# Performance work log

Measured on AMD Instinct MI355X. Metric: run time of the kernel, lower is better.

## Reference

```python
import jax, jax.numpy as jnp
import numpy as np

N_QUBITS = 7
N_LAYERS = 2
DIM = 2 ** N_QUBITS  # 128
NORM_FACTOR = 1.0


def _cnot_gather_idx(n):
    # CNOT chain (0,1),(1,2),...,(n-2,n-1) plus wraparound (n-1,0).
    # new_state[x] = old_state[idx[x]]; apply gates in reverse to arange.
    gates = [(i, i + 1) for i in range(n - 1)] + [(n - 1, 0)]
    idx = np.arange(2 ** n)
    for c, t in reversed(gates):
        cbit = 1 << (n - 1 - c)  # pennylane wire 0 = most significant bit
        tbit = 1 << (n - 1 - t)
        idx = np.where((idx & cbit) > 0, idx ^ tbit, idx)
    return jnp.asarray(idx)

CNOT_IDX = _cnot_gather_idx(N_QUBITS)


def silu(x):
    return x * jax.nn.sigmoid(x)


def cayley(A_real, A_imag):
    # Hermitianize then Cayley transform -> unitary, per layer. [L,D,D]
    A = A_real.astype(jnp.complex64) + 1j * A_imag.astype(jnp.complex64)
    A = A + jnp.conj(jnp.swapaxes(A, -1, -2))
    I = jnp.eye(DIM, dtype=A.dtype)
    return jnp.matmul(A - 1j * I, jnp.linalg.inv(A + 1j * I))


def _single_qubit_gate(theta_x, theta_y):
    # combined G = RY(theta_y) @ RX(theta_x) applied to every qubit
    cx, sx = jnp.cos(theta_x / 2), jnp.sin(theta_x / 2)
    cy, sy = jnp.cos(theta_y / 2), jnp.sin(theta_y / 2)
    RX = jnp.stack([jnp.stack([cx + 0j, -1j * sx]), jnp.stack([-1j * sx, cx + 0j])])
    RY = jnp.stack([jnp.stack([cy + 0j, -sy + 0j]), jnp.stack([sy + 0j, cy + 0j])])
    return RY @ RX


def quantum_evolve(psi, coeffs, q_mats):
    # psi: [N, DIM] complex64 normalized state vectors
    N = psi.shape[0]
    for j in range(N_LAYERS):
        psi = psi @ q_mats[j].T  # QubitUnitary: new = U @ old
        G = _single_qubit_gate(coeffs[j, 0], coeffs[j, 1])
        psi = psi.reshape((N,) + (2,) * N_QUBITS)
        for ax in range(1, N_QUBITS + 1):
            psi = jnp.moveaxis(jnp.tensordot(G, psi, axes=((1,), (ax,))), 0, ax)
        psi = psi.reshape(N, DIM)
        psi = psi[:, CNOT_IDX]  # CNOT chain is a fixed basis permutation
    return psi


def setup_inputs() -> dict:
    key = jax.random.key(0)
    ks = jax.random.split(key, 16)
    N, E = 50000, 800000
    in_nf, hid, out_nf = 128, 128, 128
    h = jax.random.normal(ks[0], (N, in_nf), dtype=jnp.float32)
    edge_index = jax.random.randint(ks[1], (2, E), 0, N)
    s = 0.05
    W_e1 = jax.random.normal(ks[2], (2 * in_nf, hid), dtype=jnp.float32) * s
    b_e1 = jnp.zeros((hid,), dtype=jnp.float32)
    W_e2 = jax.random.normal(ks[3], (hid, hid), dtype=jnp.float32) * s
    b_e2 = jnp.zeros((hid,), dtype=jnp.float32)
    W_enc = jax.random.normal(ks[4], (hid + in_nf, DIM), dtype=jnp.float32) * s
    b_enc = jnp.zeros((DIM,), dtype=jnp.float32)
    coeffs = jax.random.normal(ks[5], (N_LAYERS, 2), dtype=jnp.float32) * 0.1
    A_real = jax.random.normal(ks[6], (N_LAYERS, DIM, DIM), dtype=jnp.float32) * 0.01
    A_imag = jax.random.normal(ks[7], (N_LAYERS, DIM, DIM), dtype=jnp.float32) * 0.01
    W_dec = jax.random.normal(ks[8], (DIM, out_nf), dtype=jnp.float32) * s
    b_dec = jnp.zeros((out_nf,), dtype=jnp.float32)
    return {"h": h, "edge_index": edge_index, "W_e1": W_e1, "b_e1": b_e1,
            "W_e2": W_e2, "b_e2": b_e2, "W_enc": W_enc, "b_enc": b_enc,
            "coeffs": coeffs, "A_real": A_real, "A_imag": A_imag,
            "W_dec": W_dec, "b_dec": b_dec}


def reference(h, edge_index, W_e1, b_e1, W_e2, b_e2, W_enc, b_enc,
              coeffs, A_real, A_imag, W_dec, b_dec):
    row, col = edge_index[0], edge_index[1]
    # edge model: mij = MLP([h_src, h_tgt])
    e = jnp.concatenate([h[row], h[col]], axis=1)  # [E, 2*in_nf]
    e = silu(e @ W_e1 + b_e1)
    edge_feat = silu(e @ W_e2 + b_e2)  # [E, hid]
    # node model: scatter-sum aggregation over destination `row`
    agg = jax.ops.segment_sum(edge_feat, row, num_segments=h.shape[0]) / NORM_FACTOR
    q_input = jnp.concatenate([h, agg], axis=1) @ W_enc + b_enc  # [N, DIM]
    norm = jnp.sqrt(jnp.sum(q_input ** 2, axis=1, keepdims=True) + 1e-12)
    psi = (q_input / norm).astype(jnp.complex64)
    q_mats = cayley(A_real, A_imag)  # [L, DIM, DIM] unitary
    psi = quantum_evolve(psi, coeffs, q_mats)
    out = h + (jnp.real(psi) @ W_dec + b_dec)
    return out, edge_feat
```

## Files before the change

### kernel.cpp

```cpp
#include <hip/hip_runtime.h>
#include <math.h>

#define N_NODES 50000
#define N_EDGES 800000

typedef __attribute__((ext_vector_type(8))) short bf16x8;
typedef __attribute__((ext_vector_type(4))) short bf16x4;
typedef __attribute__((ext_vector_type(2))) short shortx2;
typedef __attribute__((ext_vector_type(4))) float f32x4;

__device__ __forceinline__ float silu_f(float x) {
    float d = 1.0f + __expf(-x);
    return x * __builtin_amdgcn_rcpf(d);
}

__device__ __forceinline__ unsigned short f2bf(float x) {
    union { float f; unsigned u; } v; v.f = x;
    unsigned r = v.u + 0x7FFFu + ((v.u >> 16) & 1u);
    return (unsigned short)(r >> 16);
}

__device__ __forceinline__ void atomic_pk_add_bf16(short* addr, shortx2 v) {
    typedef shortx2 __attribute__((address_space(1)))* gp1;
    __builtin_amdgcn_global_atomic_fadd_v2bf16((gp1)(unsigned long long)addr, v);
}

__global__ __launch_bounds__(256) void prep_kernel(const float* __restrict__ h,
                                                   short* __restrict__ hbf,
                                                   const int* __restrict__ ei,
                                                   int* __restrict__ cnt,
                                                   const float* __restrict__ A_real,
                                                   const float* __restrict__ A_imag,
                                                   float* __restrict__ H,
                                                   float* __restrict__ X) {
    const int bid = blockIdx.x;
    const int t = threadIdx.x;
    if (bid < 3125) {
        int i = bid * 256 + t;
        const float4* h4 = (const float4*)h;
        float4 v0 = h4[i * 2], v1 = h4[i * 2 + 1];
        bf16x8 b;
        b[0] = (short)f2bf(v0.x); b[1] = (short)f2bf(v0.y);
        b[2] = (short)f2bf(v0.z); b[3] = (short)f2bf(v0.w);
        b[4] = (short)f2bf(v1.x); b[5] = (short)f2bf(v1.y);
        b[6] = (short)f2bf(v1.z); b[7] = (short)f2bf(v1.w);
        ((bf16x8*)hbf)[i] = b;
        atomicAdd(&cnt[ei[i]], 1);
    } else {
        int p = bid - 3125;
        int L = p >> 2, q4 = p & 3;
        const float* ar = A_real + L * 16384;
        const float* ai = A_imag + L * 16384;
        float* hre = H + L * 32768;
        float* him = hre + 16384;
        float* xre = X + L * 32768;
        float* xim = xre + 16384;
        for (int m = 0; m < 16; ++m) {
            int idx = q4 * 4096 + t + 256 * m;
            int i = idx >> 7, j = idx & 127;
            float hr = ar[idx] + ar[j * 128 + i];
            float hi = ai[idx] - ai[j * 128 + i];
            hre[idx] = hr;
            him[idx] = hi;
            xre[idx] = hr;
            xim[idx] = hi - (i == j ? 1.0f : 0.0f);
        }
    }
}

__device__ __forceinline__ void ns_t_body(int blk, int t,
                                          const float* __restrict__ H,
                                          const float* __restrict__ X,
                                          float* __restrict__ T) {
    const int L = blk >> 4;
    const int i = (blk & 15) * 8 + (t >> 7);
    const int j = t & 127;
    const float* hre = H + L * 32768;
    const float* him = hre + 16384;
    const float* xre = X + L * 32768;
    const float* xim = xre + 16384;
    float accr = 0.f, acci = 0.f;
    #pragma unroll 4
    for (int k = 0; k < 128; ++k) {
        float hr = hre[i * 128 + k], hi = him[i * 128 + k];
        float xr = xre[k * 128 + j], xi = xim[k * 128 + j];
        accr += hr * xr - hi * xi;
        acci += hr * xi + hi * xr;
    }
    T[L * 32768 + i * 128 + j]          = accr - xim[i * 128 + j];
    T[L * 32768 + 16384 + i * 128 + j]  = acci + xre[i * 128 + j];
}

__device__ __forceinline__ void ns_x_body(int blk, int t,
                                          const float* __restrict__ X,
                                          const float* __restrict__ T,
                                          float* __restrict__ Xout) {
    const int L = blk >> 4;
    const int i = (blk & 15) * 8 + (t >> 7);
    const int j = t & 127;
    const float* xre = X + L * 32768;
    const float* xim = xre + 16384;
    const float* tre = T + L * 32768;
    const float* tim = tre + 16384;
    float accr = 0.f, acci = 0.f;
    #pragma unroll 4
    for (int k = 0; k < 128; ++k) {
        float xr = xre[i * 128 + k], xi = xim[i * 128 + k];
        float tr = tre[k * 128 + j], ti = tim[k * 128 + j];
        accr += xr * tr - xi * ti;
        acci += xr * ti + xi * tr;
    }
    Xout[L * 32768 + i * 128 + j]          = 2.0f * xre[i * 128 + j] - accr;
    Xout[L * 32768 + 16384 + i * 128 + j]  = 2.0f * xim[i * 128 + j] - acci;
}

__global__ __launch_bounds__(1024) void nst_scan_kernel(const float* __restrict__ H,
                                                        const float* __restrict__ X,
                                                        float* __restrict__ T,
                                                        const int* __restrict__ cnt,
                                                        int* __restrict__ cursor) {
    const int bid = blockIdx.x;
    const int t = threadIdx.x;
    if (bid < 32) { ns_t_body(bid, t, H, X, T); return; }
    __shared__ int sA[1024];
    __shared__ int sB[1024];
    const int CH = 49;
    int s = 0;
    #pragma unroll 4
    for (int i = 0; i < CH; ++i) {
        int idx = t * CH + i;
        if (idx < N_NODES) s += cnt[idx];
    }
    sA[t] = s;
    __syncthreads();
    int* src = sA;
    int* dst = sB;
    for (int off = 1; off < 1024; off <<= 1) {
        int v = src[t];
        if (t >= off) v += src[t - off];
        dst[t] = v;
        __syncthreads();
        int* tmp = src; src = dst; dst = tmp;
    }
    int run = (t == 0) ? 0 : src[t - 1];
    for (int i = 0; i < CH; ++i) {
        int idx = t * CH + i;
        if (idx < N_NODES) {
            cursor[idx] = run;
            run += cnt[idx];
        }
    }
}

__global__ __launch_bounds__(1024) void fill_nsx_kernel(const int* __restrict__ ei,
                                                        int* __restrict__ cursor,
                                                        int* __restrict__ elist,
                                                        const float* __restrict__ X,
                                                        const float* __restrict__ T,
                                                        float* __restrict__ Xout) {
    const int bid = blockIdx.x;
    const int t = threadIdx.x;
    if (bid < 782) {
        int e = bid * 1024 + t;
        if (e < N_EDGES) {
            int slot = atomicAdd(&cursor[ei[e]], 1);
            elist[slot] = e;
        }
        return;
    }
    ns_x_body(bid - 782, t, X, T, Xout);
}

__global__ __launch_bounds__(1024) void ns_t_kernel(const float* __restrict__ H,
                                                    const float* __restrict__ X,
                                                    float* __restrict__ T) {
    ns_t_body(blockIdx.x, threadIdx.x, H, X, T);
}

__global__ __launch_bounds__(1024) void ns_x_kernel(const float* __restrict__ X,
                                                    const float* __restrict__ T,
                                                    float* __restrict__ Xout) {
    ns_x_body(blockIdx.x, threadIdx.x, X, T, Xout);
}

__global__ __launch_bounds__(1024) void gateperm_kernel(const float* __restrict__ X,
                                                        const float* __restrict__ coeffs,
                                                        float* __restrict__ Y) {
    __shared__ float Mre[128 * 129];
    __shared__ float Mim[128 * 129];
    const int L = blockIdx.x;
    const int t = threadIdx.x;
    const float* xre = X + L * 32768;
    const float* xim = xre + 16384;

    for (int q = 0; q < 16; ++q) {
        int idx = t + 1024 * q;
        int i = idx >> 7, j = idx & 127;
        Mre[i * 129 + j] = (i == j ? 1.0f : 0.0f) + 2.0f * xim[idx];
        Mim[i * 129 + j] = -2.0f * xre[idx];
    }
    __syncthreads();

    const float tx = coeffs[2 * L + 0] * 0.5f;
    const float ty = coeffs[2 * L + 1] * 0.5f;
    const float cx = cosf(tx), sx = sinf(tx), cy = cosf(ty), sy = sinf(ty);
    const float G00r = cx * cy, G00i = sx * sy;
    const float G01r = -cx * sy, G01i = -sx * cy;
    const float G10r = cx * sy, G10i = -sx * cy;
    const float G11r = cx * cy, G11i = -sx * sy;

    for (int st = 0; st < 7; ++st) {
        int b = 1 << st;
        #pragma unroll
        for (int p = 0; p < 8; ++p) {
            int pid = t + 1024 * p;
            int col = pid & 127, ph = pid >> 7;
            int i0 = ((ph >> st) << (st + 1)) | (ph & (b - 1));
            int i1 = i0 | b;
            float v0r = Mre[i0 * 129 + col], v0i = Mim[i0 * 129 + col];
            float v1r = Mre[i1 * 129 + col], v1i = Mim[i1 * 129 + col];
            Mre[i0 * 129 + col] = G00r * v0r - G00i * v0i + G01r * v1r - G01i * v1i;
            Mim[i0 * 129 + col] = G00r * v0i + G00i * v0r + G01r * v1i + G01i * v1r;
            Mre[i1 * 129 + col] = G10r * v0r - G10i * v0i + G11r * v1r - G11i * v1i;
            Mim[i1 * 129 + col] = G10r * v0i + G10i * v0r + G11r * v1i + G11i * v1r;
        }
        __syncthreads();
    }

    const int cs[7] = {6, 5, 4, 3, 2, 1, 0};
    const int ts[7] = {0, 6, 5, 4, 3, 2, 1};
    float* yre = Y + L * 32768;
    float* yim = yre + 16384;
    for (int q = 0; q < 16; ++q) {
        int idx = t + 1024 * q;
        int ii_ = idx >> 7, col = idx & 127;
        int s = ii_;
        #pragma unroll
        for (int m = 0; m < 7; ++m) {
            int cbit = 1 << (6 - cs[m]);
            int tbit = 1 << (6 - ts[m]);
            if (s & cbit) s ^= tbit;
        }
        yre[idx] = Mre[s * 129 + col];
        yim[idx] = Mim[s * 129 + col];
    }
}

__global__ __launch_bounds__(512) void combine1_kernel(const float* __restrict__ Y,
                                                       float* __restrict__ ReM) {
    __shared__ float q1r[16384];
    __shared__ float q1i[16384];
    const int t = threadIdx.x;
    const float* q1re = Y;
    const float* q1im = Y + 16384;
    const float* q2re = Y + 32768;
    const float* q2im = Y + 49152;
    for (int q = 0; q < 32; ++q) {
        q1r[t + 512 * q] = q1re[t + 512 * q];
        q1i[t + 512 * q] = q1im[t + 512 * q];
    }
    __syncthreads();
    int i = blockIdx.x * 4 + (t >> 7);
    int j = t & 127;
    float acc = 0.f;
    for (int k = 0; k < 128; ++k) {
        acc += q2re[i * 128 + k] * q1r[k * 128 + j] - q2im[i * 128 + k] * q1i[k * 128 + j];
    }
    ReM[i * 128 + j] = acc;
}

__global__ __launch_bounds__(512) void combine2_kernel(const float* __restrict__ ReM,
                                                       const float* __restrict__ W_dec,
                                                       short* __restrict__ Dt) {
    __shared__ float ml[16384];
    __shared__ float wl[16384];
    const int t = threadIdx.x;
    for (int q = 0; q < 32; ++q) {
        ml[t + 512 * q] = ReM[t + 512 * q];
        wl[t + 512 * q] = W_dec[t + 512 * q];
    }
    __syncthreads();
    int k = blockIdx.x * 4 + (t >> 7);
    int j = t & 127;
    float acc = 0.f;
    for (int i = 0; i < 128; ++i) {
        acc += ml[i * 128 + k] * wl[i * 128 + j];
    }
    Dt[j * 128 + k] = (short)f2bf(acc);
}

__global__ __launch_bounds__(768)
__attribute__((amdgpu_waves_per_eu(3, 3)))
void edge_kernel(const short* __restrict__ hbf,
                 const int* __restrict__ ei,
                 const int* __restrict__ elist,
                 const float* __restrict__ W_e1,
                 const float* __restrict__ b_e1,
                 const float* __restrict__ W_e2,
                 const float* __restrict__ b_e2,
                 float* __restrict__ ef_out,
                 short* __restrict__ agg_bf) {
    __shared__ short w1f[64 * 64 * 8];
    __shared__ short w2f[32 * 64 * 8];
    __shared__ short c1s[12][16 * 68];

    const int t = threadIdx.x;
    const int lane = t & 63;
    const int w = t >> 6;
    const int l15 = lane & 15;
    const int kg = lane >> 4;

    {
        const float4* w1_4 = (const float4*)W_e1;
        for (int idx4 = t; idx4 < 8192; idx4 += 768) {
            int k = idx4 >> 5, j4 = idx4 & 31;
            float4 v = w1_4[idx4];
            int s = k >> 5, kgs = (k >> 3) & 3, e = k & 7;
            int fb = s * 8;
            float vz[4] = {v.x, v.y, v.z, v.w};
            #pragma unroll
            for (int z = 0; z < 4; ++z) {
                int j = j4 * 4 + z;
                int nf = j >> 4, jl = j & 15;
                w1f[((fb + nf) * 64 + kgs * 16 + jl) * 8 + e] = (short)f2bf(vz[z]);
            }
        }
        const float4* w2_4 = (const float4*)W_e2;
        for (int idx4 = t; idx4 < 4096; idx4 += 768) {
            int k = idx4 >> 5, j4 = idx4 & 31;
            float4 v = w2_4[idx4];
            int s2 = k >> 5, kgs = (k >> 3) & 3, e = k & 7;
            int fb = s2 * 8;
            float vz[4] = {v.x, v.y, v.z, v.w};
            #pragma unroll
            for (int z = 0; z < 4; ++z) {
                int j = j4 * 4 + z;
                int nf = j >> 4, jl = j & 15;
                w2f[((fb + nf) * 64 + kgs * 16 + jl) * 8 + e] = (short)f2bf(vz[z]);
            }
        }
    }
    float b1v[8], b2v[8];
    #pragma unroll
    for (int nf = 0; nf < 8; ++nf) {
        b1v[nf] = b_e1[nf * 16 + l15];
        b2v[nf] = b_e2[nf * 16 + l15];
    }
    __syncthreads();

    const bf16x8* hb8 = (const bf16x8*)hbf;
    const bf16x8* w1v = (const bf16x8*)w1f;
    const bf16x8* w2v = (const bf16x8*)w2f;
    short* myc1 = &c1s[w][0];
    const int nt = N_EDGES / 16;
    const int TW = gridDim.x * 12;
    const int wvid = blockIdx.x * 12 + w;
    int tile = (int)(((long long)nt * wvid) / TW);
    const int tend = (int)(((long long)nt * (wvid + 1)) / TW);
    if (tile >= tend) return;

    int el = elist[tile * 16 + l15];
    int ri = ei[el];
    int ci = ei[N_EDGES + el];
    bf16x8 a1[8];
    #pragma unroll
    for (int s = 0; s < 4; ++s) a1[s] = hb8[(size_t)ri * 16 + s * 4 + kg];
    #pragma unroll
    for (int s = 0; s < 4; ++s) a1[4 + s] = hb8[(size_t)ci * 16 + s * 4 + kg];

    bool hn = (tile + 1 < tend);
    int eln = 0, rin = 0, cin = 0;
    if (hn) {
        eln = elist[(tile + 1) * 16 + l15];
        rin = ei[eln];
        cin = ei[N_EDGES + eln];
    }

    float runsum[8];
    #pragma unroll
    for (int nf = 0; nf < 8; ++nf) runsum[nf] = 0.f;

    for (;;) {
        bool hn2 = (tile + 2 < tend);
        int eln2 = 0, rin2 = 0, cin2 = 0;
        if (hn2) {
            eln2 = elist[(tile + 2) * 16 + l15];
            rin2 = ei[eln2];
            cin2 = ei[N_EDGES + eln2];
        }

        f32x4 acc[8];
        #pragma unroll
        for (int nf = 0; nf < 8; ++nf) acc[nf] = (f32x4){0.f, 0.f, 0.f, 0.f};
        __builtin_amdgcn_s_setprio(1);
        #pragma unroll
        for (int s = 0; s < 8; ++s) {
            #pragma unroll
            for (int nf = 0; nf < 8; ++nf) {
                bf16x8 b = w1v[(s * 8 + nf) * 64 + lane];
                acc[nf] = __builtin_amdgcn_mfma_f32_16x16x32_bf16(a1[s], b, acc[nf], 0, 0, 0);
            }
        }
        __builtin_amdgcn_s_setprio(0);

        bf16x8 a1n[8];
        if (hn) {
            #pragma unroll
            for (int s = 0; s < 4; ++s) a1n[s] = hb8[(size_t)rin * 16 + s * 4 + kg];
            #pragma unroll
            for (int s = 0; s < 4; ++s) a1n[4 + s] = hb8[(size_t)cin * 16 + s * 4 + kg];
        }

        f32x4 acc2[8];
        #pragma unroll
        for (int nf = 0; nf < 8; ++nf) acc2[nf] = (f32x4){0.f, 0.f, 0.f, 0.f};
        #pragma unroll
        for (int half = 0; half < 2; ++half) {
            #pragma unroll
            for (int nfh = 0; nfh < 4; ++nfh) {
                int nf = half * 4 + nfh;
                #pragma unroll
                for (int r = 0; r < 4; ++r) {
                    int row = kg * 4 + r;
                    int c = nfh * 16 + l15;
                    myc1[row * 68 + c] = (short)f2bf(silu_f(acc[nf][r] + b1v[nf]));
                }
            }
            #pragma unroll
            for (int s2l = 0; s2l < 2; ++s2l) {
                int k0h = s2l * 32 + kg * 8;
                int base = l15 * 68 + k0h;
                bf16x4 lo = *(const bf16x4*)&myc1[base];
                bf16x4 hi = *(const bf16x4*)&myc1[base + 4];
                bf16x8 a2;
                #pragma unroll
                for (int z = 0; z < 4; ++z) { a2[z] = lo[z]; a2[4 + z] = hi[z]; }
                int s2 = half * 2 + s2l;
                __builtin_amdgcn_s_setprio(1);
                #pragma unroll
                for (int nf = 0; nf < 8; ++nf) {
                    bf16x8 b = w2v[(s2 * 8 + nf) * 64 + lane];
                    acc2[nf] = __builtin_amdgcn_mfma_f32_16x16x32_bf16(a2, b, acc2[nf], 0, 0, 0);
                }
                __builtin_amdgcn_s_setprio(0);
            }
        }

        int rw[4], ew[4];
        #pragma unroll
        for (int r = 0; r < 4; ++r) {
            rw[r] = __shfl(ri, kg * 4 + r);
            ew[r] = __shfl(el, kg * 4 + r);
        }
        int rwn0 = hn ? __shfl(rin, kg * 4) : -1;
        #pragma unroll
        for (int r = 0; r < 4; ++r) {
            float* efp = ef_out + (size_t)ew[r] * 128;
            #pragma unroll
            for (int nf = 0; nf < 8; ++nf) {
                int col = nf * 16 + l15;
                float v = silu_f(acc2[nf][r] + b2v[nf]);
                __builtin_nontemporal_store(v, efp + col);
                runsum[nf] += v;
            }
            bool end = (r < 3) ? (rw[r + 1] != rw[r]) : (rw[3] != rwn0);
            if (end) {
                short* agp = agg_bf + (size_t)rw[r] * 128;
                #pragma unroll
                for (int nf = 0; nf < 8; ++nf) {
                    float vn = __shfl_xor(runsum[nf], 1);
                    if ((l15 & 1) == 0) {
                        shortx2 pk;
                        pk.x = (short)f2bf(runsum[nf]);
                        pk.y = (short)f2bf(vn);
                        atomic_pk_add_bf16(agp + nf * 16 + l15, pk);
                    }
                    runsum[nf] = 0.f;
                }
            }
        }

        if (!hn) break;
        tile += 1;
        el = eln; ri = rin; ci = cin;
        #pragma unroll
        for (int s = 0; s < 8; ++s) a1[s] = a1n[s];
        hn = hn2; eln = eln2; rin = rin2; cin = cin2;
    }
}

__global__ __launch_bounds__(1024)
__attribute__((amdgpu_waves_per_eu(4, 4)))
void node_kernel(const short* __restrict__ hbf,
                 const short* __restrict__ agg_bf,
                 const float* __restrict__ W_enc,
                 const float* __restrict__ b_enc,
                 const short* __restrict__ Dt_bf,
                 const float* __restrict__ b_dec,
                 const float* __restrict__ h,
                 float* __restrict__ out) {
    __shared__ short wef[64 * 64 * 8];
    __shared__ short dtf[32 * 64 * 8];
    __shared__ short c1s[16][16 * 68];

    const int t = threadIdx.x;
    const int lane = t & 63;
    const int w = t >> 6;
    const int l15 = lane & 15;
    const int kg = lane >> 4;

    {
        const float4* we4 = (const float4*)W_enc;
        for (int idx4 = t; idx4 < 8192; idx4 += 1024) {
            int k = idx4 >> 5, j4 = idx4 & 31;
            float4 v = we4[idx4];
            int s = k >> 5, kgs = (k >> 3) & 3, e = k & 7;
            int fb = s * 8;
            float vz[4] = {v.x, v.y, v.z, v.w};
            #pragma unroll
            for (int z = 0; z < 4; ++z) {
                int j = j4 * 4 + z;
                int nf = j >> 4, jl = j & 15;
                wef[((fb + nf) * 64 + kgs * 16 + jl) * 8 + e] = (short)f2bf(vz[z]);
            }
        }
        const bf16x8* dt8 = (const bf16x8*)Dt_bf;
        bf16x8* dtv = (bf16x8*)dtf;
        for (int idx8 = t; idx8 < 2048; idx8 += 1024) {
            int brow = idx8 >> 4, kslot = idx8 & 15;
            int s2 = kslot >> 2, kgs = kslot & 3;
            int nf = brow >> 4, jl = brow & 15;
            dtv[(s2 * 8 + nf) * 64 + kgs * 16 + jl] = dt8[idx8];
        }
    }
    float bj1[8], bj2[8];
    #pragma unroll
    for (int nf = 0; nf < 8; ++nf) {
        bj1[nf] = b_enc[nf * 16 + l15];
        bj2[nf] = b_dec[nf * 16 + l15];
    }
    __syncthreads();

    const bf16x8* hb8 = (const bf16x8*)hbf;
    const bf16x8* ab8 = (const bf16x8*)agg_bf;
    const bf16x8* wev = (const bf16x8*)wef;
    const bf16x8* dtv = (const bf16x8*)dtf;
    short* myc1 = &c1s[w][0];
    const int nt = N_NODES / 16;
    const int tile = blockIdx.x * 16 + w;
    if (tile >= nt) return;

    const int node = tile * 16 + l15;
    bf16x8 a[8];
    #pragma unroll
    for (int s = 0; s < 4; ++s) a[s] = hb8[(size_t)node * 16 + s * 4 + kg];
    #pragma unroll
    for (int s = 0; s < 4; ++s) a[4 + s] = ab8[(size_t)node * 16 + s * 4 + kg];

    f32x4 acc[8];
    #pragma unroll
    for (int nf = 0; nf < 8; ++nf) acc[nf] = (f32x4){0.f, 0.f, 0.f, 0.f};
    __builtin_amdgcn_s_setprio(1);
    #pragma unroll
    for (int s = 0; s < 8; ++s) {
        #pragma unroll
        for (int nf = 0; nf < 8; ++nf) {
            bf16x8 b = wev[(s * 8 + nf) * 64 + lane];
            acc[nf] = __builtin_amdgcn_mfma_f32_16x16x32_bf16(a[s], b, acc[nf], 0, 0, 0);
        }
    }
    __builtin_amdgcn_s_setprio(0);

    float nr[4] = {0.f, 0.f, 0.f, 0.f};
    #pragma unroll
    for (int nf = 0; nf < 8; ++nf) {
        #pragma unroll
        for (int r = 0; r < 4; ++r) {
            acc[nf][r] += bj1[nf];
            nr[r] += acc[nf][r] * acc[nf][r];
        }
    }
    #pragma unroll
    for (int r = 0; r < 4; ++r) {
        nr[r] += __shfl_xor(nr[r], 1);
        nr[r] += __shfl_xor(nr[r], 2);
        nr[r] += __shfl_xor(nr[r], 4);
        nr[r] += __shfl_xor(nr[r], 8);
        nr[r] = 1.0f / sqrtf(nr[r] + 1e-12f);
    }

    f32x4 acc2[8];
    #pragma unroll
    for (int nf = 0; nf < 8; ++nf) acc2[nf] = (f32x4){0.f, 0.f, 0.f, 0.f};
    #pragma unroll
    for (int half = 0; half < 2; ++half) {
        #pragma unroll
        for (int nfh = 0; nfh < 4; ++nfh) {
            int nf = half * 4 + nfh;
            #pragma unroll
            for (int r = 0; r < 4; ++r) {
                int row = kg * 4 + r;
                int c = nfh * 16 + l15;
                myc1[row * 68 + c] = (short)f2bf(acc[nf][r] * nr[r]);
            }
        }
        #pragma unroll
        for (int s2l = 0; s2l < 2; ++s2l) {
            int k0h = s2l * 32 + kg * 8;
            int base = l15 * 68 + k0h;
            bf16x4 lo = *(const bf16x4*)&myc1[base];
            bf16x4 hi = *(const bf16x4*)&myc1[base + 4];
            bf16x8 a2;
            #pragma unroll
            for (int z = 0; z < 4; ++z) { a2[z] = lo[z]; a2[4 + z] = hi[z]; }
            int s2 = half * 2 + s2l;
            __builtin_amdgcn_s_setprio(1);
            #pragma unroll
            for (int nf = 0; nf < 8; ++nf) {
                bf16x8 b = dtv[(s2 * 8 + nf) * 64 + lane];
                acc2[nf] = __builtin_amdgcn_mfma_f32_16x16x32_bf16(a2, b, acc2[nf], 0, 0, 0);
            }
            __builtin_amdgcn_s_setprio(0);
        }
    }

    #pragma unroll
    for (int r = 0; r < 4; ++r) {
        size_t rowb = (size_t)(tile * 16 + kg * 4 + r) * 128;
        #pragma unroll
        for (int nf = 0; nf < 8; ++nf) {
            int col = nf * 16 + l15;
            out[rowb + col] = h[rowb + col] + acc2[nf][r] + bj2[nf];
        }
    }
}

extern "C" void kernel_launch(void* const* d_in, const int* in_sizes, int n_in,
                              void* d_out, int out_size, void* d_ws, size_t ws_size,
                              hipStream_t stream) {
    const float* h      = (const float*)d_in[0];
    const int*   ei     = (const int*)d_in[1];
    const float* W_e1   = (const float*)d_in[2];
    const float* b_e1   = (const float*)d_in[3];
    const float* W_e2   = (const float*)d_in[4];
    const float* b_e2   = (const float*)d_in[5];
    const float* W_enc  = (const float*)d_in[6];
    const float* b_enc  = (const float*)d_in[7];
    const float* coeffs = (const float*)d_in[8];
    const float* A_real = (const float*)d_in[9];
    const float* A_imag = (const float*)d_in[10];
    const float* W_dec  = (const float*)d_in[11];
    const float* b_dec  = (const float*)d_in[12];

    float* out    = (float*)d_out;
    float* ef_out = out + (size_t)N_NODES * 128;

    short* agg_bf = (short*)d_ws;
    int*   cnt    = (int*)(agg_bf + (size_t)N_NODES * 128);
    short* h_bf   = (short*)(cnt + 50176);
    int*   cursor = (int*)(h_bf + (size_t)N_NODES * 128);
    int*   elist  = cursor + 50176;
    float* small  = (float*)(elist + N_EDGES);
    float* Ybuf   = small;
    float* ReM    = Ybuf + 65536;
    float* Hbuf   = ReM + 16384;
    float* Xa     = Hbuf + 65536;
    float* Xb     = Xa + 65536;
    float* Tbuf   = Xb + 65536;
    short* Dt_bf  = (short*)(Tbuf + 65536);

    hipMemsetAsync(agg_bf, 0, (size_t)N_NODES * 128 * sizeof(short) + 50176 * sizeof(int),
                   stream);

    prep_kernel<<<3133, 256, 0, stream>>>(h, h_bf, ei, cnt, A_real, A_imag, Hbuf, Xa);
    nst_scan_kernel<<<33, 1024, 0, stream>>>(Hbuf, Xa, Tbuf, cnt, cursor);
    fill_nsx_kernel<<<814, 1024, 0, stream>>>(ei, cursor, elist, Xa, Tbuf, Xb);
    ns_t_kernel<<<32, 1024, 0, stream>>>(Hbuf, Xb, Tbuf);
    ns_x_kernel<<<32, 1024, 0, stream>>>(Xb, Tbuf, Xa);

    gateperm_kernel<<<2, 1024, 0, stream>>>(Xa, coeffs, Ybuf);
    combine1_kernel<<<32, 512, 0, stream>>>(Ybuf, ReM);
    combine2_kernel<<<32, 512, 0, stream>>>(ReM, W_dec, Dt_bf);

    edge_kernel<<<256, 768, 0, stream>>>(h_bf, ei, elist, W_e1, b_e1, W_e2, b_e2,
                                         ef_out, agg_bf);

    node_kernel<<<196, 1024, 0, stream>>>(h_bf, agg_bf, W_enc, b_enc, Dt_bf, b_dec, h, out);
}
```

Baseline: 592.8 us.

## Overlap quantum-matrix chain with edge MLP in one persistent kernel

Merges the Newton-Schulz iterations, gate/permutation, and two combine matmuls into the edge kernel. Blocks 224-255 run that small dependent chain, separated by global atomic spin barriers, then process a reduced share of edge tiles. Blocks 0-223 start edge work at once. This removes five small serial launches and their idle tail by overlapping them with edge compute. The risk is deadlock if the 32 chain blocks are not co-resident, and load imbalance from the fixed tile split.

Result: slower. 711.0 us (+19.9%).

```diff
diff --git a/kernel.cpp b/kernel.cpp
--- a/kernel.cpp
+++ b/kernel.cpp
@@ -3,6 +3,11 @@
 
 #define N_NODES 50000
 #define N_EDGES 800000
+
+#define EDGE_MAIN_BLOCKS 224
+#define MAIN_TILES 198
+#define MAIN_TOTAL (EDGE_MAIN_BLOCKS * MAIN_TILES)
+#define DC_TOTAL (N_EDGES / 16 - MAIN_TOTAL)
 
 typedef __attribute__((ext_vector_type(8))) short bf16x8;
 typedef __attribute__((ext_vector_type(4))) short bf16x4;
@@ -23,6 +28,19 @@
 __device__ __forceinline__ void atomic_pk_add_bf16(short* addr, shortx2 v) {
     typedef shortx2 __attribute__((address_space(1)))* gp1;
     __builtin_amdgcn_global_atomic_fadd_v2bf16((gp1)(unsigned long long)addr, v);
+}
+
+__device__ __forceinline__ void dbar(int* ctr, int target) {
+    __threadfence();
+    __syncthreads();
+    if (threadIdx.x == 0) {
+        __hip_atomic_fetch_add(ctr, 1, __ATOMIC_RELEASE, __HIP_MEMORY_SCOPE_AGENT);
+        while (__hip_atomic_load(ctr, __ATOMIC_RELAXED, __HIP_MEMORY_SCOPE_AGENT) < target) {
+            __builtin_amdgcn_s_sleep(2);
+        }
+    }
+    __syncthreads();
+    __threadfence();
 }
 
 __global__ __launch_bounds__(256) void prep_kernel(const float* __restrict__ h,
@@ -171,144 +189,145 @@
     ns_x_body(bid - 782, t, X, T, Xout);
 }
 
-__global__ __launch_bounds__(1024) void ns_t_kernel(const float* __restrict__ H,
-                                                    const float* __restrict__ X,
-                                                    float* __restrict__ T) {
-    ns_t_body(blockIdx.x, threadIdx.x, H, X, T);
-}
-
-__global__ __launch_bounds__(1024) void ns_x_kernel(const float* __restrict__ X,
-                                                    const float* __restrict__ T,
-                                                    float* __restrict__ Xout) {
-    ns_x_body(blockIdx.x, threadIdx.x, X, T, Xout);
-}
-
-__global__ __launch_bounds__(1024) void gateperm_kernel(const float* __restrict__ X,
-                                                        const float* __restrict__ coeffs,
-                                                        float* __restrict__ Y) {
-    __shared__ float Mre[128 * 129];
-    __shared__ float Mim[128 * 129];
-    const int L = blockIdx.x;
-    const int t = threadIdx.x;
-    const float* xre = X + L * 32768;
-    const float* xim = xre + 16384;
-
-    for (int q = 0; q < 16; ++q) {
-        int idx = t + 1024 * q;
-        int i = idx >> 7, j = idx & 127;
-        Mre[i * 129 + j] = (i == j ? 1.0f : 0.0f) + 2.0f * xim[idx];
-        Mim[i * 129 + j] = -2.0f * xre[idx];
-    }
-    __syncthreads();
-
-    const float tx = coeffs[2 * L + 0] * 0.5f;
-    const float ty = coeffs[2 * L + 1] * 0.5f;
-    const float cx = cosf(tx), sx = sinf(tx), cy = cosf(ty), sy = sinf(ty);
-    const float G00r = cx * cy, G00i = sx * sy;
-    const float G01r = -cx * sy, G01i = -sx * cy;
-    const float G10r = cx * sy, G10i = -sx * cy;
-    const float G11r = cx * cy, G11i = -sx * sy;
-
-    for (int st = 0; st < 7; ++st) {
-        int b = 1 << st;
-        #pragma unroll
-        for (int p = 0; p < 8; ++p) {
-            int pid = t + 1024 * p;
-            int col = pid & 127, ph = pid >> 7;
-            int i0 = ((ph >> st) << (st + 1)) | (ph & (b - 1));
-            int i1 = i0 | b;
-            float v0r = Mre[i0 * 129 + col], v0i = Mim[i0 * 129 + col];
-            float v1r = Mre[i1 * 129 + col], v1i = Mim[i1 * 129 + col];
-            Mre[i0 * 129 + col] = G00r * v0r - G00i * v0i + G01r * v1r - G01i * v1i;
-            Mim[i0 * 129 + col] = G00r * v0i + G00i * v0r + G01r * v1i + G01i * v1r;
-            Mre[i1 * 129 + col] = G10r * v0r - G10i * v0i + G11r * v1r - G11i * v1i;
-            Mim[i1 * 129 + col] = G10r * v0i + G10i * v0r + G11r * v1i + G11i * v1r;
-        }
-        __syncthreads();
-    }
-
-    const int cs[7] = {6, 5, 4, 3, 2, 1, 0};
-    const int ts[7] = {0, 6, 5, 4, 3, 2, 1};
-    float* yre = Y + L * 32768;
-    float* yim = yre + 16384;
-    for (int q = 0; q < 16; ++q) {
-        int idx = t + 1024 * q;
-        int ii_ = idx >> 7, col = idx & 127;
-        int s = ii_;
-        #pragma unroll
-        for (int m = 0; m < 7; ++m) {
-            int cbit = 1 << (6 - cs[m]);
-            int tbit = 1 << (6 - ts[m]);
-            if (s & cbit) s ^= tbit;
-        }
-        yre[idx] = Mre[s * 129 + col];
-        yim[idx] = Mim[s * 129 + col];
-    }
-}
-
-__global__ __launch_bounds__(512) void combine1_kernel(const float* __restrict__ Y,
-                                                       float* __restrict__ ReM) {
-    __shared__ float q1r[16384];
-    __shared__ float q1i[16384];
-    const int t = threadIdx.x;
-    const float* q1re = Y;
-    const float* q1im = Y + 16384;
-    const float* q2re = Y + 32768;
-    const float* q2im = Y + 49152;
-    for (int q = 0; q < 32; ++q) {
-        q1r[t + 512 * q] = q1re[t + 512 * q];
-        q1i[t + 512 * q] = q1im[t + 512 * q];
-    }
-    __syncthreads();
-    int i = blockIdx.x * 4 + (t >> 7);
-    int j = t & 127;
-    float acc = 0.f;
-    for (int k = 0; k < 128; ++k) {
-        acc += q2re[i * 128 + k] * q1r[k * 128 + j] - q2im[i * 128 + k] * q1i[k * 128 + j];
-    }
-    ReM[i * 128 + j] = acc;
-}
-
-__global__ __launch_bounds__(512) void combine2_kernel(const float* __restrict__ ReM,
-                                                       const float* __restrict__ W_dec,
-                                                       short* __restrict__ Dt) {
-    __shared__ float ml[16384];
-    __shared__ float wl[16384];
-    const int t = threadIdx.x;
-    for (int q = 0; q < 32; ++q) {
-        ml[t + 512 * q] = ReM[t + 512 * q];
-        wl[t + 512 * q] = W_dec[t + 512 * q];
-    }
-    __syncthreads();
-    int k = blockIdx.x * 4 + (t >> 7);
-    int j = t & 127;
-    float acc = 0.f;
-    for (int i = 0; i < 128; ++i) {
-        acc += ml[i * 128 + k] * wl[i * 128 + j];
-    }
-    Dt[j * 128 + k] = (short)f2bf(acc);
-}
-
 __global__ __launch_bounds__(768)
 __attribute__((amdgpu_waves_per_eu(3, 3)))
-void edge_kernel(const short* __restrict__ hbf,
-                 const int* __restrict__ ei,
-                 const int* __restrict__ elist,
-                 const float* __restrict__ W_e1,
-                 const float* __restrict__ b_e1,
-                 const float* __restrict__ W_e2,
-                 const float* __restrict__ b_e2,
-                 float* __restrict__ ef_out,
-                 short* __restrict__ agg_bf) {
-    __shared__ short w1f[64 * 64 * 8];
-    __shared__ short w2f[32 * 64 * 8];
-    __shared__ short c1s[12][16 * 68];
-
+void edge_dchain_kernel(const short* __restrict__ hbf,
+                        const int* __restrict__ ei,
+                        const int* __restrict__ elist,
+                        const float* __restrict__ W_e1,
+                        const float* __restrict__ b_e1,
+                        const float* __restrict__ W_e2,
+                        const float* __restrict__ b_e2,
+                        float* __restrict__ ef_out,
+                        short* __restrict__ agg_bf,
+                        const float* __restrict__ H,
+                        const float* __restrict__ Xb,
+                        float* __restrict__ T,
+                        float* __restrict__ Xa,
+                        const float* __restrict__ coeffs,
+                        float* __restrict__ Y,
+                        float* __restrict__ ReM,
+                        const float* __restrict__ W_dec,
+                        short* __restrict__ Dt,
+                        int* __restrict__ ctr) {
+    __shared__ __align__(16) char smraw[133120];
+    short* w1f = (short*)smraw;
+    short* w2f = (short*)(smraw + 65536);
+    short* c1s = (short*)(smraw + 98304);
+    float* smf = (float*)smraw;
+
+    const int bid = blockIdx.x;
     const int t = threadIdx.x;
     const int lane = t & 63;
     const int w = t >> 6;
     const int l15 = lane & 15;
     const int kg = lane >> 4;
+
+    int tstart, tstop;
+    if (bid < EDGE_MAIN_BLOCKS) {
+        tstart = bid * MAIN_TILES;
+        tstop  = tstart + MAIN_TILES;
+    } else {
+        const int db = bid - EDGE_MAIN_BLOCKS;
+        for (int idx = t; idx < 1024; idx += 768) ns_t_body(db, idx, H, Xb, T);
+        dbar(ctr + 0, 32);
+        for (int idx = t; idx < 1024; idx += 768) ns_x_body(db, idx, Xb, T, Xa);
+        dbar(ctr + 1, 32);
+        if (db < 2) {
+            float* Mre = smf;
+            float* Mim = smf + 128 * 129;
+            const float* xre = Xa + db * 32768;
+            const float* xim = xre + 16384;
+            for (int idx = t; idx < 16384; idx += 768) {
+                int i = idx >> 7, j = idx & 127;
+                Mre[i * 129 + j] = (i == j ? 1.0f : 0.0f) + 2.0f * xim[idx];
+                Mim[i * 129 + j] = -2.0f * xre[idx];
+            }
+            __syncthreads();
+            const float tx = coeffs[2 * db + 0] * 0.5f;
+            const float ty = coeffs[2 * db + 1] * 0.5f;
+            const float cx = cosf(tx), sx = sinf(tx), cy = cosf(ty), sy = sinf(ty);
+            const float G00r = cx * cy, G00i = sx * sy;
+            const float G01r = -cx * sy, G01i = -sx * cy;
+            const float G10r = cx * sy, G10i = -sx * cy;
+            const float G11r = cx * cy, G11i = -sx * sy;
+            for (int st = 0; st < 7; ++st) {
+                int b = 1 << st;
+                for (int pid = t; pid < 8192; pid += 768) {
+                    int col = pid & 127, ph = pid >> 7;
+                    int i0 = ((ph >> st) << (st + 1)) | (ph & (b - 1));
+                    int i1 = i0 | b;
+                    float v0r = Mre[i0 * 129 + col], v0i = Mim[i0 * 129 + col];
+                    float v1r = Mre[i1 * 129 + col], v1i = Mim[i1 * 129 + col];
+                    Mre[i0 * 129 + col] = G00r * v0r - G00i * v0i + G01r * v1r - G01i * v1i;
+                    Mim[i0 * 129 + col] = G00r * v0i + G00i * v0r + G01r * v1i + G01i * v1r;
+                    Mre[i1 * 129 + col] = G10r * v0r - G10i * v0i + G11r * v1r - G11i * v1i;
+                    Mim[i1 * 129 + col] = G10r * v0i + G10i * v0r + G11r * v1i + G11i * v1r;
+                }
+                __syncthreads();
+            }
+            const int cs[7] = {6, 5, 4, 3, 2, 1, 0};
+            const int ts[7] = {0, 6, 5, 4, 3, 2, 1};
+            float* yre = Y + db * 32768;
+            float* yim = yre + 16384;
+            for (int idx = t; idx < 16384; idx += 768) {
+                int ii_ = idx >> 7, col = idx & 127;
+                int s = ii_;
+                #pragma unroll
+                for (int m = 0; m < 7; ++m) {
+                    int cbit = 1 << (6 - cs[m]);
+                    int tbit = 1 << (6 - ts[m]);
+                    if (s & cbit) s ^= tbit;
+                }
+                yre[idx] = Mre[s * 129 + col];
+                yim[idx] = Mim[s * 129 + col];
+            }
+        }
+        dbar(ctr + 2, 32);
+        {
+            float* q1r = smf;
+            float* q1i = smf + 16384;
+            for (int idx = t; idx < 16384; idx += 768) {
+                q1r[idx] = Y[idx];
+                q1i[idx] = Y[16384 + idx];
+            }
+            __syncthreads();
+            if (t < 512) {
+                int o = db * 512 + t;
+                int i = o >> 7, j = o & 127;
+                const float* q2re = Y + 32768;
+                const float* q2im = Y + 49152;
+                float acc = 0.f;
+                for (int k = 0; k < 128; ++k) {
+                    acc += q2re[i * 128 + k] * q1r[k * 128 + j]
+                         - q2im[i * 128 + k] * q1i[k * 128 + j];
+                }
+                ReM[o] = acc;
+            }
+        }
+        dbar(ctr + 3, 32);
+        {
+            float* ml = smf;
+            float* wl = smf + 16384;
+            for (int idx = t; idx < 16384; idx += 768) {
+                ml[idx] = ReM[idx];
+                wl[idx] = W_dec[idx];
+            }
+            __syncthreads();
+            if (t < 512) {
+                int o = db * 512 + t;
+                int k = o >> 7, j = o & 127;
+                float acc = 0.f;
+                for (int i = 0; i < 128; ++i) {
+                    acc += ml[i * 128 + k] * wl[i * 128 + j];
+                }
+                Dt[j * 128 + k] = (short)f2bf(acc);
+            }
+            __syncthreads();
+        }
+        tstart = MAIN_TOTAL + (DC_TOTAL * db) / 32;
+        tstop  = MAIN_TOTAL + (DC_TOTAL * (db + 1)) / 32;
+    }
 
     {
         const float4* w1_4 = (const float4*)W_e1;
@@ -351,12 +370,10 @@
     const bf16x8* hb8 = (const bf16x8*)hbf;
     const bf16x8* w1v = (const bf16x8*)w1f;
     const bf16x8* w2v = (const bf16x8*)w2f;
-    short* myc1 = &c1s[w][0];
-    const int nt = N_EDGES / 16;
-    const int TW = gridDim.x * 12;
-    const int wvid = blockIdx.x * 12 + w;
-    int tile = (int)(((long long)nt * wvid) / TW);
-    const int tend = (int)(((long long)nt * (wvid + 1)) / TW);
+    short* myc1 = &c1s[w * 1088];
+    const int span = tstop - tstart;
+    int tile = tstart + (span * w) / 12;
+    const int tend = tstart + (span * (w + 1)) / 12;
     if (tile >= tend) return;
 
     int el = elist[tile * 16 + l15];
@@ -657,7 +674,8 @@
 
     short* agg_bf = (short*)d_ws;
     int*   cnt    = (int*)(agg_bf + (size_t)N_NODES * 128);
-    short* h_bf   = (short*)(cnt + 50176);
+    int*   ctr    = cnt + 50176;
+    short* h_bf   = (short*)(ctr + 16);
     int*   cursor = (int*)(h_bf + (size_t)N_NODES * 128);
     int*   elist  = cursor + 50176;
     float* small  = (float*)(elist + N_EDGES);
@@ -669,21 +687,18 @@
     float* Tbuf   = Xb + 65536;
     short* Dt_bf  = (short*)(Tbuf + 65536);
 
-    hipMemsetAsync(agg_bf, 0, (size_t)N_NODES * 128 * sizeof(short) + 50176 * sizeof(int),
+    hipMemsetAsync(agg_bf, 0,
+                   (size_t)N_NODES * 128 * sizeof(short) + 50176 * sizeof(int) + 64,
                    stream);
 
     prep_kernel<<<3133, 256, 0, stream>>>(h, h_bf, ei, cnt, A_real, A_imag, Hbuf, Xa);
     nst_scan_kernel<<<33, 1024, 0, stream>>>(Hbuf, Xa, Tbuf, cnt, cursor);
     fill_nsx_kernel<<<814, 1024, 0, stream>>>(ei, cursor, elist, Xa, Tbuf, Xb);
-    ns_t_kernel<<<32, 1024, 0, stream>>>(Hbuf, Xb, Tbuf);
-    ns_x_kernel<<<32, 1024, 0, stream>>>(Xb, Tbuf, Xa);
-
-    gateperm_kernel<<<2, 1024, 0, stream>>>(Xa, coeffs, Ybuf);
-    combine1_kernel<<<32, 512, 0, stream>>>(Ybuf, ReM);
-    combine2_kernel<<<32, 512, 0, stream>>>(ReM, W_dec, Dt_bf);
-
-    edge_kernel<<<256, 768, 0, stream>>>(h_bf, ei, elist, W_e1, b_e1, W_e2, b_e2,
-                                         ef_out, agg_bf);
+
+    edge_dchain_kernel<<<256, 768, 0, stream>>>(h_bf, ei, elist, W_e1, b_e1, W_e2, b_e2,
+                                                ef_out, agg_bf,
+                                                Hbuf, Xb, Tbuf, Xa, coeffs, Ybuf, ReM,
+                                                W_dec, Dt_bf, ctr);
 
     node_kernel<<<196, 1024, 0, stream>>>(h_bf, agg_bf, W_enc, b_enc, Dt_bf, b_dec, h, out);
 }
```
